# Kernel optimization log

Hardware: AMD Instinct MI355X
Metric: run time of the kernel (lower is better)

## Reference

```python
import jax, jax.numpy as jnp
import numpy as np
import math

N = 500_000
C_IN = 16
C_OUT = 64
H, W = 256, 256
PE_DIM = 32
BOUNDS = (-1.0, 1.0)
LN_EPS = 1e-5


def setup_inputs() -> dict:
    key = jax.random.key(0)
    ks = jax.random.split(key, 4)
    d_in = C_IN + 6 * PE_DIM  # 208
    pos = jax.random.uniform(ks[0], (N, 3), jnp.float32, minval=-1.0, maxval=1.0)
    features = jax.random.normal(ks[1], (N, C_IN), jnp.float32)
    W1 = jax.random.normal(ks[2], (d_in, C_OUT), jnp.float32) * (1.0 / math.sqrt(d_in))
    b1 = jnp.zeros((C_OUT,), jnp.float32)
    ln_g = jnp.ones((C_OUT,), jnp.float32)
    ln_b = jnp.zeros((C_OUT,), jnp.float32)
    W2 = jax.random.normal(ks[3], (C_OUT, C_OUT), jnp.float32) * (1.0 / math.sqrt(C_OUT))
    b2 = jnp.zeros((C_OUT,), jnp.float32)
    return {"pos": pos, "features": features, "W1": W1, "b1": b1,
            "ln_g": ln_g, "ln_b": ln_b, "W2": W2, "b2": b2,
            "axis1": 0, "axis2": 1}


def _pos_encode(pos):
    # sinusoidal encoding: per spatial dim, sin/cos at PE_DIM frequencies
    scale = BOUNDS[1] - BOUNDS[0]
    freq_bands = jnp.arange(PE_DIM, dtype=jnp.float32) / PE_DIM  # linspace(0,31,32)/32
    freqs = (pos / scale)[..., None] * (2.0 ** freq_bands) * math.pi  # [N,3,PE]
    # ordering per dim: sin_d, cos_d -> [N, 3*2*PE]
    enc = jnp.stack([jnp.sin(freqs), jnp.cos(freqs)], axis=2)  # [N,3,2,PE]
    return enc.reshape(pos.shape[0], 3 * 2 * PE_DIM)


def _layernorm(x, g, b):
    mu = jnp.mean(x, axis=-1, keepdims=True)
    var = jnp.var(x, axis=-1, keepdims=True)
    return (x - mu) * jax.lax.rsqrt(var + LN_EPS) * g + b


def reference(pos, features, W1, b1, ln_g, ln_b, W2, b2, axis1, axis2):
    # MLP on [features | pos_encoding]
    combined = jnp.concatenate([features, _pos_encode(pos)], axis=-1)  # [N,208]
    h = combined @ W1 + b1
    h = jax.nn.gelu(_layernorm(h, ln_g, ln_b), approximate=False)
    feat = h @ W2 + b2  # [N,C_OUT]

    # grid indices for the projected plane
    lo, hi = BOUNDS
    norm = jnp.clip((pos - lo) / (hi - lo), 0.0, 1.0)
    res = jnp.array([H, W], jnp.float32)
    i1 = jnp.clip(jnp.floor(norm[:, axis1] * res[0]), 0, H - 1).astype(jnp.int32)
    i2 = jnp.clip(jnp.floor(norm[:, axis2] * res[1]), 0, W - 1).astype(jnp.int32)
    flat = i1 * W + i2  # [N]

    # scatter-mean into grid
    sums = jax.ops.segment_sum(feat, flat, num_segments=H * W)  # [H*W, C]
    counts = jax.ops.segment_sum(jnp.ones((feat.shape[0],), jnp.float32), flat,
                                 num_segments=H * W)
    grid = sums / jnp.maximum(counts, 1.0)[:, None]  # [H*W, C]
    grid = grid.reshape(H, W, C_OUT).transpose(2, 0, 1)  # [C,H,W]
    return grid[None]  # [1,C,H,W]
```

## Files before the change

### kernel.cpp

```cpp
#include <hip/hip_runtime.h>
#include <math.h>

#define NPTS   500000
#define CIN    16
#define COUT   64
#define GRID_W 256
#define NCELL  65536
#define BCAP   32

#define WS_HIST   0
#define WS_BUCKET 262144
#define WS_WPK    8650752
#define WS_FEAT   8687616
#define WS_NEED   (WS_FEAT + (size_t)NPTS * COUT * 2)

#define MB_BLOCKS ((NPTS + 511) / 512)

#define W_HALFS   18432
#define W1_FRAGS  28

typedef _Float16 f16x8 __attribute__((ext_vector_type(8)));
typedef _Float16 f16x2 __attribute__((ext_vector_type(2)));
typedef float    f32x4 __attribute__((ext_vector_type(4)));

__device__ __forceinline__ f16x2 pk2(float a, float b) {
    auto r = __builtin_amdgcn_cvt_pkrtz(a, b);
    union { decltype(r) x; f16x2 y; } u; u.x = r;
    return u.y;
}

__device__ __forceinline__ float vsin(float x) {
    float r;
    asm("v_sin_f32 %0, %1" : "=v"(r) : "v"(x));
    return r;
}

__device__ __forceinline__ float vexp2(float x) {
    float r;
    asm("v_exp_f32 %0, %1" : "=v"(r) : "v"(x));
    return r;
}

__device__ __forceinline__ int cell_index(float v) {
    float nf = fminf(fmaxf((v + 1.0f) * 0.5f, 0.0f), 1.0f);
    int i = (int)floorf(nf * 256.0f);
    return i > 255 ? 255 : i;
}

__device__ __forceinline__ int flat_of(const float* pos, int p, int a1, int a2) {
    float pa1 = pos[p * 3 + a1];
    float pa2 = pos[p * 3 + a2];
    return cell_index(pa1) * GRID_W + cell_index(pa2);
}

__global__ __launch_bounds__(256)
void pack_w_hist0_kernel(const float* __restrict__ W1,
                         const float* __restrict__ W2,
                         _Float16* __restrict__ wpk,
                         unsigned int* __restrict__ hist)
{
    int i = blockIdx.x * 256 + threadIdx.x;
    if (i < W_HALFS) {
        int j = i & 7, lane = (i >> 3) & 63, f = i >> 9;
        int k  = ((f < W1_FRAGS) ? (f >> 2) : ((f - W1_FRAGS) >> 2)) * 32 + ((lane >> 4) << 3) + j;
        int ch = (f & 3) * 16 + (lane & 15);
        float v;
        if (f < W1_FRAGS) v = (k < 208) ? W1[k * 64 + ch] : 0.0f;
        else              v = W2[k * 64 + ch];
        wpk[i] = (_Float16)v;
    }
    hist[i] = 0u;
}

__global__ __launch_bounds__(512, 4)
void mlp_mfma_kernel(const float* __restrict__ pos,
                     const float* __restrict__ feats,
                     const _Float16* __restrict__ wpk,
                     const float* __restrict__ b1,
                     const float* __restrict__ ln_g,
                     const float* __restrict__ ln_b,
                     const int*   __restrict__ ax1p,
                     const int*   __restrict__ ax2p,
                     unsigned int* __restrict__ hist,
                     int* __restrict__ bucket,
                     _Float16* __restrict__ featbuf,
                     float* __restrict__ out,
                     int use_feat)
{
    __shared__ __align__(16) _Float16 WF[W_HALFS];
    __shared__ __align__(16) _Float16 PS[8 * 1024];

    {
        const uint4* src = (const uint4*)wpk;
        uint4* dst = (uint4*)WF;
        for (int i = threadIdx.x; i < W_HALFS / 8; i += 512) dst[i] = src[i];
    }

    const int lane = threadIdx.x & 63;
    const int wv   = threadIdx.x >> 6;
    const int g    = lane >> 4;
    const int n    = lane & 15;
    char* Pw = (char*)(PS + wv * 1024);
    const unsigned sw = (unsigned)((n & 7) << 4);

    const int wbase = blockIdx.x * 512 + wv * 64;
    const int a1 = ax1p[0], a2 = ax2p[0];

    const float base  = 0.25f * exp2f((float)((8 * g + 16) & 31) * 0.03125f);
    const float RSTEP = 1.02189714865411668f;

    __syncthreads();

    #pragma unroll 1
    for (int tp = 0; tp < 2; ++tp) {
        float px[2], py[2], pz[2];
        f16x8 fH[2];
        #pragma unroll
        for (int u = 0; u < 2; ++u) {
            const int st = wbase + (tp * 2 + u) * 16 + n;
            const int p  = (st < NPTS) ? st : 0;
            px[u] = pos[3 * p + 0];
            py[u] = pos[3 * p + 1];
            pz[u] = pos[3 * p + 2];
            if (g < 2) {
                const float4* fr = (const float4*)(feats + (size_t)p * CIN + g * 8);
                float4 fa = fr[0], fb = fr[1];
                union { f16x8 v; f16x2 h[4]; } Uf;
                Uf.h[0] = pk2(fa.x, fa.y); Uf.h[1] = pk2(fa.z, fa.w);
                Uf.h[2] = pk2(fb.x, fb.y); Uf.h[3] = pk2(fb.z, fb.w);
                fH[u] = Uf.v;
            }
        }

        f32x4 acc[2][4];
        #pragma unroll
        for (int u = 0; u < 2; ++u)
            #pragma unroll
            for (int c = 0; c < 4; ++c)
                acc[u][c] = (f32x4){0.0f, 0.0f, 0.0f, 0.0f};

        #pragma unroll
        for (int s = 0; s < 7; ++s) {
            f16x8 U[2];
            const int k0 = s * 32 + g * 8;
            if (s == 0 && g < 2) {
                U[0] = fH[0]; U[1] = fH[1];
            } else if (k0 >= 208) {
                union { f16x8 v; f16x2 h[4]; } Z;
                #pragma unroll
                for (int q = 0; q < 4; ++q) Z.h[q] = pk2(0.0f, 0.0f);
                U[0] = Z.v; U[1] = Z.v;
            } else {
                const int   e    = k0 - 16;
                const float off  = (e & 32) ? 0.25f : 0.0f;
                const float offc = (e & 32) ? (0.25f * (1.0f - RSTEP)) : 0.0f;
                #pragma unroll
                for (int u = 0; u < 2; ++u) {
                    const float pv = (e < 64) ? px[u] : ((e < 128) ? py[u] : pz[u]);
                    float a = fmaf(pv, base, off);
                    union { f16x8 v; f16x2 h[4]; } G;
                    #pragma unroll
                    for (int q = 0; q < 4; ++q) {
                        float v0 = vsin(a); a = fmaf(a, RSTEP, offc);
                        float v1 = vsin(a); a = fmaf(a, RSTEP, offc);
                        G.h[q] = pk2(v0, v1);
                    }
                    U[u] = G.v;
                }
            }
            #pragma unroll
            for (int c = 0; c < 4; ++c) {
                f16x8 af = ((const f16x8*)WF)[(s * 4 + c) * 64 + lane];
                acc[0][c] = __builtin_amdgcn_mfma_f32_16x16x32_f16(af, U[0], acc[0][c], 0, 0, 0);
                acc[1][c] = __builtin_amdgcn_mfma_f32_16x16x32_f16(af, U[1], acc[1][c], 0, 0, 0);
            }
        }

        #pragma unroll
        for (int u = 0; u < 2; ++u) {
            float s1 = 0.0f, s2 = 0.0f;
            #pragma unroll
            for (int c = 0; c < 4; ++c) {
                f32x4 b1q = *(const f32x4*)(b1 + 16 * c + 4 * g);
                #pragma unroll
                for (int r = 0; r < 4; ++r) {
                    float x = acc[u][c][r] + b1q[r];
                    acc[u][c][r] = x;
                    s1 += x; s2 += x * x;
                }
            }
            s1 += __shfl_xor(s1, 16); s2 += __shfl_xor(s2, 16);
            s1 += __shfl_xor(s1, 32); s2 += __shfl_xor(s2, 32);
            const float mu   = s1 * (1.0f / 64.0f);
            const float var  = s2 * (1.0f / 64.0f) - mu * mu;
            const float rstd = __builtin_amdgcn_rsqf(var + 1e-5f);

            #pragma unroll
            for (int c = 0; c < 4; ++c) {
                f32x4 gq = *(const f32x4*)(ln_g + 16 * c + 4 * g);
                f32x4 bq = *(const f32x4*)(ln_b + 16 * c + 4 * g);
                float gv[4];
                #pragma unroll
                for (int r = 0; r < 4; ++r) {
                    float x  = (acc[u][c][r] - mu) * rstd * gq[r] + bq[r];
                    float w  = x * (2.30211812f + 0.10295203f * x * x);
                    float e2 = vexp2(w);
                    gv[r] = x * e2 * __builtin_amdgcn_rcpf(e2 + 1.0f);
                }
                union { f16x2 h[2]; uint2 u2; } W;
                W.h[0] = pk2(gv[0], gv[1]);
                W.h[1] = pk2(gv[2], gv[3]);
                *(uint2*)(Pw + n * 128 + (((unsigned)(32 * c + 8 * g)) ^ sw)) = W.u2;
            }

            f32x4 acc2[4];
            #pragma unroll
            for (int c = 0; c < 4; ++c) acc2[c] = (f32x4){0.0f, 0.0f, 0.0f, 0.0f};
            #pragma unroll
            for (int s = 0; s < 2; ++s) {
                f16x8 bf2 = *(const f16x8*)(Pw + n * 128 + (((unsigned)(64 * s + 16 * g)) ^ sw));
                #pragma unroll
                for (int c = 0; c < 4; ++c) {
                    f16x8 af = ((const f16x8*)WF)[(W1_FRAGS + s * 4 + c) * 64 + lane];
                    acc2[c] = __builtin_amdgcn_mfma_f32_16x16x32_f16(af, bf2, acc2[c], 0, 0, 0);
                }
            }

            if (use_feat) {
                const int gs = wbase + (tp * 2 + u) * 16 + n;
                if (gs < NPTS) {
                    _Float16* dstp = featbuf + (size_t)gs * COUT + 4 * g;
                    #pragma unroll
                    for (int c = 0; c < 4; ++c) {
                        union { f16x2 h[2]; uint2 u2; } W;
                        W.h[0] = pk2(acc2[c][0], acc2[c][1]);
                        W.h[1] = pk2(acc2[c][2], acc2[c][3]);
                        *(uint2*)(dstp + 16 * c) = W.u2;
                    }
                }
            } else {
                const int st = wbase + (tp * 2 + u) * 16 + n;
                if (st < NPTS) {
                    const int cellr = flat_of(pos, st, ax1p[0], ax2p[0]);
                    #pragma unroll
                    for (int c = 0; c < 4; ++c)
                        #pragma unroll
                        for (int r = 0; r < 4; ++r)
                            unsafeAtomicAdd(&out[(size_t)(16 * c + 4 * g + r) * NCELL + cellr],
                                            acc2[c][r]);
                }
            }
        }

        {
            const int st2 = wbase + (tp * 2 + (g & 1)) * 16 + n;
            if (g < 2 && st2 < NPTS) {
                const float qx = (g & 1) ? px[1] : px[0];
                const float qy = (g & 1) ? py[1] : py[0];
                const float qz = (g & 1) ? pz[1] : pz[0];
                const float pa1 = (a1 == 0) ? qx : ((a1 == 1) ? qy : qz);
                const float pa2 = (a2 == 0) ? qx : ((a2 == 1) ? qy : qz);
                const int flat = cell_index(pa1) * GRID_W + cell_index(pa2);
                const unsigned int old = atomicAdd(&hist[flat], 1u);
                if (bucket && old < BCAP) bucket[flat * BCAP + (int)old] = st2;
            }
        }
    }
}

__global__ __launch_bounds__(1024)
void reduce_kernel(const _Float16* __restrict__ featbuf,
                   const int* __restrict__ bucket,
                   const unsigned int* __restrict__ hist,
                   const float* __restrict__ b2,
                   float* __restrict__ out)
{
    __shared__ float R[16][66];
    const int lane  = threadIdx.x & 63;
    const int wv    = threadIdx.x >> 6;
    const int cbase = blockIdx.x * 16;
    const int cq    = lane & 7;
    const int rsl   = lane >> 3;

    const int cell = cbase + wv;
    const unsigned int cnt  = hist[cell];
    const unsigned int cntu = cnt < BCAP ? cnt : BCAP;
    const int bbase = cell * BCAP;

    float acc[8];
    #pragma unroll
    for (int j = 0; j < 8; ++j) acc[j] = 0.0f;

    for (unsigned int k = 0; k < cntu; k += 8) {
        const unsigned int kk = k + (unsigned int)rsl;
        const bool ok = kk < cntu;
        const int r = bucket[bbase + (int)(ok ? kk : 0u)];
        union { uint4 u; f16x2 h[4]; } V;
        V.u = *(const uint4*)(featbuf + (size_t)r * COUT + cq * 8);
        #pragma unroll
        for (int j = 0; j < 4; ++j) {
            acc[2 * j]     += ok ? (float)V.h[j].x : 0.0f;
            acc[2 * j + 1] += ok ? (float)V.h[j].y : 0.0f;
        }
    }
    #pragma unroll
    for (int m = 8; m <= 32; m <<= 1)
        #pragma unroll
        for (int j = 0; j < 8; ++j)
            acc[j] += __shfl_xor(acc[j], m);

    if (rsl == 0) {
        const float inv = 1.0f / fmaxf((float)cnt, 1.0f);
        float4 b2a = *(const float4*)(b2 + cq * 8);
        float4 b2b = *(const float4*)(b2 + cq * 8 + 4);
        const float bb[8] = {b2a.x, b2a.y, b2a.z, b2a.w, b2b.x, b2b.y, b2b.z, b2b.w};
        #pragma unroll
        for (int j = 0; j < 8; ++j)
            R[wv][cq * 8 + j] = cnt ? (acc[j] * inv + bb[j]) : 0.0f;
    }
    __syncthreads();

    const int ch = threadIdx.x >> 4;
    const int ci = threadIdx.x & 15;
    out[ch * NCELL + cbase + ci] = R[ci][ch];
}

__global__ void finalize_kernel(float* __restrict__ out,
                                const unsigned int* __restrict__ hist,
                                const float* __restrict__ b2)
{
    int t = blockIdx.x * 256 + threadIdx.x;
    int cell = t & (NCELL - 1);
    int ch   = t >> 16;
    float c  = (float)hist[cell];
    out[t] = out[t] / fmaxf(c, 1.0f) + ((c > 0.0f) ? b2[ch] : 0.0f);
}

extern "C" void kernel_launch(void* const* d_in, const int* in_sizes, int n_in,
                              void* d_out, int out_size, void* d_ws, size_t ws_size,
                              hipStream_t stream) {
    (void)in_sizes; (void)n_in; (void)out_size;
    const float* pos   = (const float*)d_in[0];
    const float* feats = (const float*)d_in[1];
    const float* W1    = (const float*)d_in[2];
    const float* b1    = (const float*)d_in[3];
    const float* ln_g  = (const float*)d_in[4];
    const float* ln_b  = (const float*)d_in[5];
    const float* W2    = (const float*)d_in[6];
    const float* b2    = (const float*)d_in[7];
    const int*   ax1   = (const int*)d_in[8];
    const int*   ax2   = (const int*)d_in[9];

    char* ws = (char*)d_ws;
    unsigned int* hist   = (unsigned int*)(ws + WS_HIST);
    int*          bucket = (int*)(ws + WS_BUCKET);
    _Float16*     wpk    = (_Float16*)(ws + WS_WPK);
    _Float16*     featbf = (_Float16*)(ws + WS_FEAT);

    float* out = (float*)d_out;
    const int use_feat = (ws_size >= WS_NEED) ? 1 : 0;

    if (!use_feat)
        hipMemsetAsync(d_out, 0, (size_t)COUT * NCELL * sizeof(float), stream);

    pack_w_hist0_kernel<<<256, 256, 0, stream>>>(W1, W2, wpk, hist);
    mlp_mfma_kernel<<<MB_BLOCKS, 512, 0, stream>>>(
        pos, feats, wpk, b1, ln_g, ln_b, ax1, ax2, hist,
        use_feat ? bucket : (int*)nullptr, featbf, out, use_feat);
    if (use_feat)
        reduce_kernel<<<NCELL / 16, 1024, 0, stream>>>(featbf, bucket, hist, b2, out);
    else
        finalize_kernel<<<(COUT * NCELL) / 256, 256, 0, stream>>>(out, hist, b2);
}
```

Before: 188.1 us.

## Fuse weight packing into MLP kernel, memset histogram, two cells per wave in reduce

Drops the separate weight-pack kernel: each MLP block now converts W1/W2 from fp32 global into the fp16 fragment layout in shared memory itself, and the histogram is zeroed with a memset instead. The reduce kernel now runs 512 threads per block, with each wave gathering two cells at once to get more loads in flight. The cost is redundant fp32 weight reads and conversion in each of roughly a thousand MLP blocks, replacing a small one-off pack pass.

```diff
diff --git a/kernel.cpp b/kernel.cpp
--- a/kernel.cpp
+++ b/kernel.cpp
@@ -10,8 +10,7 @@
 
 #define WS_HIST   0
 #define WS_BUCKET 262144
-#define WS_WPK    8650752
-#define WS_FEAT   8687616
+#define WS_FEAT   8650752
 #define WS_NEED   (WS_FEAT + (size_t)NPTS * COUT * 2)
 
 #define MB_BLOCKS ((NPTS + 511) / 512)
@@ -53,29 +52,11 @@
     return cell_index(pa1) * GRID_W + cell_index(pa2);
 }
 
-__global__ __launch_bounds__(256)
-void pack_w_hist0_kernel(const float* __restrict__ W1,
-                         const float* __restrict__ W2,
-                         _Float16* __restrict__ wpk,
-                         unsigned int* __restrict__ hist)
-{
-    int i = blockIdx.x * 256 + threadIdx.x;
-    if (i < W_HALFS) {
-        int j = i & 7, lane = (i >> 3) & 63, f = i >> 9;
-        int k  = ((f < W1_FRAGS) ? (f >> 2) : ((f - W1_FRAGS) >> 2)) * 32 + ((lane >> 4) << 3) + j;
-        int ch = (f & 3) * 16 + (lane & 15);
-        float v;
-        if (f < W1_FRAGS) v = (k < 208) ? W1[k * 64 + ch] : 0.0f;
-        else              v = W2[k * 64 + ch];
-        wpk[i] = (_Float16)v;
-    }
-    hist[i] = 0u;
-}
-
 __global__ __launch_bounds__(512, 4)
 void mlp_mfma_kernel(const float* __restrict__ pos,
                      const float* __restrict__ feats,
-                     const _Float16* __restrict__ wpk,
+                     const float* __restrict__ W1,
+                     const float* __restrict__ W2,
                      const float* __restrict__ b1,
                      const float* __restrict__ ln_g,
                      const float* __restrict__ ln_b,
@@ -90,10 +71,14 @@
     __shared__ __align__(16) _Float16 WF[W_HALFS];
     __shared__ __align__(16) _Float16 PS[8 * 1024];
 
-    {
-        const uint4* src = (const uint4*)wpk;
-        uint4* dst = (uint4*)WF;
-        for (int i = threadIdx.x; i < W_HALFS / 8; i += 512) dst[i] = src[i];
+    for (int i = threadIdx.x; i < W_HALFS; i += 512) {
+        int j = i & 7, ln = (i >> 3) & 63, f = i >> 9;
+        int k  = ((f < W1_FRAGS) ? (f >> 2) : ((f - W1_FRAGS) >> 2)) * 32 + ((ln >> 4) << 3) + j;
+        int ch = (f & 3) * 16 + (ln & 15);
+        float v;
+        if (f < W1_FRAGS) v = (k < 208) ? W1[k * 64 + ch] : 0.0f;
+        else              v = W2[k * 64 + ch];
+        WF[i] = (_Float16)v;
     }
 
     const int lane = threadIdx.x & 63;
@@ -241,7 +226,7 @@
             } else {
                 const int st = wbase + (tp * 2 + u) * 16 + n;
                 if (st < NPTS) {
-                    const int cellr = flat_of(pos, st, ax1p[0], ax2p[0]);
+                    const int cellr = flat_of(pos, st, a1, a2);
                     #pragma unroll
                     for (int c = 0; c < 4; ++c)
                         #pragma unroll
@@ -268,7 +253,7 @@
     }
 }
 
-__global__ __launch_bounds__(1024)
+__global__ __launch_bounds__(512)
 void reduce_kernel(const _Float16* __restrict__ featbuf,
                    const int* __restrict__ bucket,
                    const unsigned int* __restrict__ hist,
@@ -277,52 +262,68 @@
 {
     __shared__ float R[16][66];
     const int lane  = threadIdx.x & 63;
-    const int wv    = threadIdx.x >> 6;
+    const int wvid  = threadIdx.x >> 6;
     const int cbase = blockIdx.x * 16;
     const int cq    = lane & 7;
     const int rsl   = lane >> 3;
 
-    const int cell = cbase + wv;
-    const unsigned int cnt  = hist[cell];
-    const unsigned int cntu = cnt < BCAP ? cnt : BCAP;
-    const int bbase = cell * BCAP;
-
-    float acc[8];
+    const int c0 = cbase + wvid * 2;
+    const int c1 = c0 + 1;
+    const unsigned int cnt0 = hist[c0], cnt1 = hist[c1];
+    const unsigned int cu0 = cnt0 < BCAP ? cnt0 : BCAP;
+    const unsigned int cu1 = cnt1 < BCAP ? cnt1 : BCAP;
+    const int bb0 = c0 * BCAP, bb1 = c1 * BCAP;
+
+    float a0[8], a1v[8];
     #pragma unroll
-    for (int j = 0; j < 8; ++j) acc[j] = 0.0f;
-
-    for (unsigned int k = 0; k < cntu; k += 8) {
+    for (int j = 0; j < 8; ++j) { a0[j] = 0.0f; a1v[j] = 0.0f; }
+
+    const unsigned int kmax = cu0 > cu1 ? cu0 : cu1;
+    for (unsigned int k = 0; k < kmax; k += 8) {
         const unsigned int kk = k + (unsigned int)rsl;
-        const bool ok = kk < cntu;
-        const int r = bucket[bbase + (int)(ok ? kk : 0u)];
-        union { uint4 u; f16x2 h[4]; } V;
-        V.u = *(const uint4*)(featbuf + (size_t)r * COUT + cq * 8);
+        const bool ok0 = kk < cu0;
+        const bool ok1 = kk < cu1;
+        int r0 = bucket[bb0 + (int)(ok0 ? kk : 0u)];
+        int r1 = bucket[bb1 + (int)(ok1 ? kk : 0u)];
+        r0 = ok0 ? r0 : 0;
+        r1 = ok1 ? r1 : 0;
+        union { uint4 u; f16x2 h[4]; } V0, V1;
+        V0.u = *(const uint4*)(featbuf + (size_t)r0 * COUT + cq * 8);
+        V1.u = *(const uint4*)(featbuf + (size_t)r1 * COUT + cq * 8);
         #pragma unroll
         for (int j = 0; j < 4; ++j) {
-            acc[2 * j]     += ok ? (float)V.h[j].x : 0.0f;
-            acc[2 * j + 1] += ok ? (float)V.h[j].y : 0.0f;
+            a0[2 * j]      += ok0 ? (float)V0.h[j].x : 0.0f;
+            a0[2 * j + 1]  += ok0 ? (float)V0.h[j].y : 0.0f;
+            a1v[2 * j]     += ok1 ? (float)V1.h[j].x : 0.0f;
+            a1v[2 * j + 1] += ok1 ? (float)V1.h[j].y : 0.0f;
         }
     }
     #pragma unroll
     for (int m = 8; m <= 32; m <<= 1)
         #pragma unroll
-        for (int j = 0; j < 8; ++j)
-            acc[j] += __shfl_xor(acc[j], m);
+        for (int j = 0; j < 8; ++j) {
+            a0[j]  += __shfl_xor(a0[j], m);
+            a1v[j] += __shfl_xor(a1v[j], m);
+        }
 
     if (rsl == 0) {
-        const float inv = 1.0f / fmaxf((float)cnt, 1.0f);
         float4 b2a = *(const float4*)(b2 + cq * 8);
         float4 b2b = *(const float4*)(b2 + cq * 8 + 4);
         const float bb[8] = {b2a.x, b2a.y, b2a.z, b2a.w, b2b.x, b2b.y, b2b.z, b2b.w};
-        #pragma unroll
-        for (int j = 0; j < 8; ++j)
-            R[wv][cq * 8 + j] = cnt ? (acc[j] * inv + bb[j]) : 0.0f;
+        const float i0 = 1.0f / fmaxf((float)cnt0, 1.0f);
+        const float i1 = 1.0f / fmaxf((float)cnt1, 1.0f);
+        #pragma unroll
+        for (int j = 0; j < 8; ++j) {
+            R[wvid * 2 + 0][cq * 8 + j] = cnt0 ? (a0[j]  * i0 + bb[j]) : 0.0f;
+            R[wvid * 2 + 1][cq * 8 + j] = cnt1 ? (a1v[j] * i1 + bb[j]) : 0.0f;
+        }
     }
     __syncthreads();
 
-    const int ch = threadIdx.x >> 4;
-    const int ci = threadIdx.x & 15;
-    out[ch * NCELL + cbase + ci] = R[ci][ch];
+    const int ch = threadIdx.x >> 3;
+    const int ci = threadIdx.x & 7;
+    out[ch * NCELL + cbase + ci]     = R[ci][ch];
+    out[ch * NCELL + cbase + ci + 8] = R[ci + 8][ch];
 }
 
 __global__ void finalize_kernel(float* __restrict__ out,
@@ -354,21 +355,20 @@
     char* ws = (char*)d_ws;
     unsigned int* hist   = (unsigned int*)(ws + WS_HIST);
     int*          bucket = (int*)(ws + WS_BUCKET);
-    _Float16*     wpk    = (_Float16*)(ws + WS_WPK);
     _Float16*     featbf = (_Float16*)(ws + WS_FEAT);
 
     float* out = (float*)d_out;
     const int use_feat = (ws_size >= WS_NEED) ? 1 : 0;
 
+    hipMemsetAsync(hist, 0, NCELL * sizeof(unsigned int), stream);
     if (!use_feat)
         hipMemsetAsync(d_out, 0, (size_t)COUT * NCELL * sizeof(float), stream);
 
-    pack_w_hist0_kernel<<<256, 256, 0, stream>>>(W1, W2, wpk, hist);
     mlp_mfma_kernel<<<MB_BLOCKS, 512, 0, stream>>>(
-        pos, feats, wpk, b1, ln_g, ln_b, ax1, ax2, hist,
+        pos, feats, W1, W2, b1, ln_g, ln_b, ax1, ax2, hist,
         use_feat ? bucket : (int*)nullptr, featbf, out, use_feat);
     if (use_feat)
-        reduce_kernel<<<NCELL / 16, 1024, 0, stream>>>(featbf, bucket, hist, b2, out);
+        reduce_kernel<<<NCELL / 16, 512, 0, stream>>>(featbf, bucket, hist, b2, out);
     else
         finalize_kernel<<<(COUT * NCELL) / 256, 256, 0, stream>>>(out, hist, b2);
 }
```

Result: slower. 197.1 us (+4.8%).
